# Kernel optimization log

Measured on AMD Instinct MI355X. Metric: run time of the kernel, lower is better.

## Reference

```python
import jax, jax.numpy as jnp
import numpy as np

N_DRUG = 2000
N_REL = 100
N_TAIL = 50000
E = 500_000
D = 128
SAMPLE = 64
BN_EPS = 1e-5


def setup_inputs() -> dict:
    key = jax.random.key(0)
    ks = jax.random.split(key, 12)
    xav = lambda k, shape: jax.random.normal(k, shape, jnp.float32) * np.float32(np.sqrt(2.0 / (shape[0] + shape[-1])))
    return {
        'drug_emb': xav(ks[0], (N_DRUG, D)),
        'rel_emb': xav(ks[1], (N_REL, D)),
        'tail_emb': xav(ks[2], (N_TAIL, D)),
        'w1': xav(ks[3], (D, D)),
        'b1': jnp.zeros((D,), jnp.float32),
        'w2': xav(ks[4], (D, D)),
        'b2': jnp.zeros((D,), jnp.float32),
        'fc2_w': xav(ks[5], (D, 2 * D)),
        'fc2_b': jnp.zeros((D,), jnp.float32),
        'gamma': jnp.ones((D,), jnp.float32),
        'beta': jnp.zeros((D,), jnp.float32),
        'x': jax.random.normal(ks[6], (N_DRUG, D), jnp.float32),
        'dkg_head': jnp.sort(jax.random.randint(ks[7], (E,), 0, N_DRUG, jnp.int32)),
        'dkg_rel': jax.random.randint(ks[8], (E,), 0, N_REL, jnp.int32),
        'dkg_tail': jax.random.randint(ks[9], (E,), 0, N_TAIL, jnp.int32),
        'sample_size': SAMPLE,
    }


def reference(drug_emb, rel_emb, tail_emb, w1, b1, w2, b2, fc2_w, fc2_b,
              gamma, beta, x, dkg_head, dkg_rel, dkg_tail, sample_size):
    n_drug, d = drug_emb.shape
    n_edges = dkg_head.shape[0]
    # per-edge semantic score: MLP(drug[h] * rel[r]) summed over feature dim
    had = drug_emb[dkg_head] * rel_emb[dkg_rel]            # [E, D]
    h = jax.nn.sigmoid(had @ w1.T + b1)                    # [E, D]
    score = jnp.sum(h @ w2.T + b2, axis=1, keepdims=True)  # [E, 1]
    temp = score * tail_emb[dkg_tail]                      # [E, D]
    # per-head sampling without replacement: keep at most sample_size edges
    # per drug (edges are sorted by head; rank = position within head group).
    starts = jnp.searchsorted(dkg_head, jnp.arange(n_drug, dtype=dkg_head.dtype))
    rank = jnp.arange(n_edges) - starts[dkg_head]
    keep = (rank < sample_size).astype(temp.dtype)[:, None]
    neigh = jax.ops.segment_sum(temp * keep, dkg_head, num_segments=n_drug)  # [N, D]
    # fullConnectionLayer2: Linear(2D -> D) + BatchNorm1d (training stats)
    concat = jnp.concatenate([drug_emb, neigh], axis=1)    # [N, 2D]
    out = concat @ fc2_w.T + fc2_b                         # [N, D]
    mean = jnp.mean(out, axis=0)
    var = jnp.var(out, axis=0)
    out = (out - mean) * jax.lax.rsqrt(var + BN_EPS) * gamma + beta
    return (out, x)
```

## Files before the change

### kernel.cpp

```cpp
#include <hip/hip_runtime.h>
#include <hip/hip_bf16.h>


#define D 128

typedef __attribute__((ext_vector_type(8))) short bf16x8;
typedef __attribute__((ext_vector_type(8))) unsigned short u16x8;
typedef __attribute__((ext_vector_type(4))) float f32x4;
typedef __attribute__((ext_vector_type(4))) unsigned short u16x4;

__device__ __forceinline__ unsigned short f2bf(float f) {
  union { float f; unsigned int u; } v; v.f = f;
  unsigned int r = v.u + 0x7FFFu + ((v.u >> 16) & 1u);
  return (unsigned short)(r >> 16);
}

__global__ void prep_kernel(const float* __restrict__ w1,
                            const float* __restrict__ w2,
                            const float* __restrict__ b2,
                            const float* __restrict__ drug_emb,
                            const float* __restrict__ fc2_w,
                            const float* __restrict__ x,
                            const int* __restrict__ head,
                            unsigned short* __restrict__ w1b,
                            unsigned short* __restrict__ drugb,
                            unsigned short* __restrict__ fc2wb,
                            int* __restrict__ starts,
                            float* __restrict__ w2s,
                            float* __restrict__ b2sum,
                            float* __restrict__ out_hi,
                            float* __restrict__ bnacc,
                            int* __restrict__ counter,
                            int E_total, int n_drug, int total) {
  int g = blockIdx.x * 256 + threadIdx.x;
  if (g < E_total) {
    int h1 = head[g];
    int h0 = (g == 0) ? -1 : head[g - 1];
    for (int d = h0 + 1; d <= h1; ++d) starts[d] = g;
    if (g == E_total - 1) {
      for (int d = h1 + 1; d <= n_drug; ++d) starts[d] = E_total;
    }
  }
  if (g < D * D) w1b[g] = f2bf(w1[g]);
  if (g < 2 * D * D) fc2wb[g] = f2bf(fc2_w[g]);
  if (g < n_drug * D) drugb[g] = f2bf(drug_emb[g]);
  if (g < total) out_hi[g] = x[g];
  if (g < 2 * D) bnacc[g] = 0.f;
  if (g == 2 * D) *counter = 0;
  if (g < D) {
    float s0=0.f,s1=0.f,s2=0.f,s3=0.f,s4=0.f,s5=0.f,s6=0.f,s7=0.f;
    #pragma unroll
    for (int j = 0; j < D; j += 8) {
      s0 += w2[(j+0)*D+g]; s1 += w2[(j+1)*D+g];
      s2 += w2[(j+2)*D+g]; s3 += w2[(j+3)*D+g];
      s4 += w2[(j+4)*D+g]; s5 += w2[(j+5)*D+g];
      s6 += w2[(j+6)*D+g]; s7 += w2[(j+7)*D+g];
    }
    w2s[g] = ((s0+s1)+(s2+s3))+((s4+s5)+(s6+s7));
  }
  if (g < 64) {
    float v = b2[g] + b2[g + 64];
    v += __shfl_xor(v, 1);  v += __shfl_xor(v, 2);  v += __shfl_xor(v, 4);
    v += __shfl_xor(v, 8);  v += __shfl_xor(v, 16); v += __shfl_xor(v, 32);
    if (g == 0) b2sum[0] = v;
  }
}

__global__ __launch_bounds__(256, 2) void edge_kernel(
    const float* __restrict__ drug_emb, const float* __restrict__ rel_emb,
    const float* __restrict__ tail_emb, const float* __restrict__ b1,
    const int* __restrict__ dkg_rel, const int* __restrict__ dkg_tail,
    const int* __restrict__ starts, const unsigned short* __restrict__ w1b,
    const float* __restrict__ w2s, const float* __restrict__ b2sum,
    const int* __restrict__ samp, unsigned short* __restrict__ neighb) {
  const int n = blockIdx.x;
  const int tid = threadIdx.x;
  const int w = tid >> 6, lane = tid & 63;
  const int fl = lane & 15, kh = lane >> 4;
  const int g = tid >> 5, l5 = tid & 31;

  __shared__ __align__(16) unsigned short hadb[64][136];
  __shared__ float scorePart[4][64];
  __shared__ float scoreL[64];
  __shared__ int   tails[64];
  __shared__ int   relIdx[64];
  float* gpart = (float*)&hadb[0][0];

  const int base = starts[n];
  const int end  = starts[n + 1];
  int ss = samp[0]; if (ss > 64) ss = 64;
  int cnt = end - base; if (cnt > ss) cnt = ss; if (cnt < 0) cnt = 0;

  if (tid < 64) {
    tails[tid]  = (tid < cnt) ? dkg_tail[base + tid] : 0;
    relIdx[tid] = (tid < cnt) ? dkg_rel[base + tid] : 0;
  }

  const f32x4 dr = *(const f32x4*)(drug_emb + (long)n * D + l5 * 4);

  bf16x8 bfr[2][4];
  float w2sr[2], b1r[2];
  #pragma unroll
  for (int jq = 0; jq < 2; ++jq) {
    int f = (w * 2 + jq) * 16 + fl;
    w2sr[jq] = w2s[f];
    b1r[jq]  = b1[f];
    #pragma unroll
    for (int kt = 0; kt < 4; ++kt)
      bfr[jq][kt] = *(const bf16x8*)(w1b + f * D + kt * 32 + kh * 8);
  }
  const float b2s = b2sum[0];

  __syncthreads();

  #pragma unroll
  for (int it = 0; it < 8; ++it) {
    int e = it * 8 + g;
    int r = relIdx[e];
    f32x4 rl = *(const f32x4*)(rel_emb + (long)r * D + l5 * 4);
    f32x4 v = dr * rl;
    u16x4 pk = { f2bf(v.x), f2bf(v.y), f2bf(v.z), f2bf(v.w) };
    *(u16x4*)&hadb[e][l5 * 4] = pk;
  }

  f32x4 trow[8];
  #pragma unroll
  for (int it = 0; it < 8; ++it) {
    int e = it * 8 + g;
    trow[it] = *(const f32x4*)(tail_emb + (long)tails[e] * D + l5 * 4);
  }

  __syncthreads();

  f32x4 acc[4][2];
  #pragma unroll
  for (int mt = 0; mt < 4; ++mt)
    #pragma unroll
    for (int jq = 0; jq < 2; ++jq)
      acc[mt][jq] = (f32x4){b1r[jq], b1r[jq], b1r[jq], b1r[jq]};

  #pragma unroll
  for (int kt = 0; kt < 4; ++kt) {
    bf16x8 af[4];
    #pragma unroll
    for (int mt = 0; mt < 4; ++mt)
      af[mt] = *(const bf16x8*)&hadb[mt * 16 + fl][kt * 32 + kh * 8];
    #pragma unroll
    for (int mt = 0; mt < 4; ++mt)
      #pragma unroll
      for (int jq = 0; jq < 2; ++jq)
        acc[mt][jq] = __builtin_amdgcn_mfma_f32_16x16x32_bf16(af[mt], bfr[jq][kt], acc[mt][jq], 0, 0, 0);
  }

  #pragma unroll
  for (int mt = 0; mt < 4; ++mt) {
    #pragma unroll
    for (int r = 0; r < 4; ++r) {
      float p = 0.f;
      #pragma unroll
      for (int jq = 0; jq < 2; ++jq) {
        float hh = 1.f / (1.f + __expf(-acc[mt][jq][r]));
        p += hh * w2sr[jq];
      }
      p += __shfl_xor(p, 1);
      p += __shfl_xor(p, 2);
      p += __shfl_xor(p, 4);
      p += __shfl_xor(p, 8);
      if (fl == 0) scorePart[w][mt * 16 + kh * 4 + r] = p;
    }
  }
  __syncthreads();

  if (tid < 64) {
    float sc = scorePart[0][tid] + scorePart[1][tid] + scorePart[2][tid] + scorePart[3][tid] + b2s;
    scoreL[tid] = (tid < cnt) ? sc : 0.f;
  }
  __syncthreads();

  f32x4 a = (f32x4){0.f, 0.f, 0.f, 0.f};
  #pragma unroll
  for (int it = 0; it < 8; ++it) {
    int e = it * 8 + g;
    float s = scoreL[e];
    a += trow[it] * s;
  }
  ((f32x4*)gpart)[g * 32 + l5] = a;
  __syncthreads();

  if (tid < D) {
    float s = 0.f;
    #pragma unroll
    for (int q = 0; q < 8; ++q) s += gpart[q * 128 + tid];
    neighb[(long)n * D + tid] = f2bf(s);
  }
}

__global__ __launch_bounds__(256, 1) void fc2bn_kernel(
    const unsigned short* __restrict__ drugb, const unsigned short* __restrict__ neighb,
    const unsigned short* __restrict__ fc2wb, const float* __restrict__ fc2_b,
    const float* __restrict__ gamma, const float* __restrict__ beta,
    float* __restrict__ bnacc, int* __restrict__ counter,
    float* __restrict__ out, int n_drug, int nblocks) {
  const int tid = threadIdx.x;
  const int w = tid >> 6, lane = tid & 63;
  const int fl = lane & 15, kh = lane >> 4;
  const int n0 = blockIdx.x * 64;

  __shared__ __align__(16) unsigned short asmem[64][264];

  #pragma unroll
  for (int it = 0; it < 8; ++it) {
    int c = it * 256 + tid;
    int row = c >> 5;
    int off = (c & 31) * 16;
    int gr = n0 + row;
    u16x8 v = (u16x8){0,0,0,0,0,0,0,0};
    if (gr < n_drug) {
      const unsigned short* src = (off < 256) ? (drugb + (long)gr * D + (off >> 1))
                                              : (neighb + (long)gr * D + ((off - 256) >> 1));
      v = *(const u16x8*)src;
    }
    *(u16x8*)((char*)&asmem[0][0] + row * 528 + off) = v;
  }

  bf16x8 bfr[2][8];
  float bjr[2];
  #pragma unroll
  for (int jq = 0; jq < 2; ++jq) {
    int f = (w * 2 + jq) * 16 + fl;
    bjr[jq] = fc2_b[f];
    #pragma unroll
    for (int kt = 0; kt < 8; ++kt)
      bfr[jq][kt] = *(const bf16x8*)(fc2wb + (long)f * 256 + kt * 32 + kh * 8);
  }
  __syncthreads();

  f32x4 acc[4][2];
  #pragma unroll
  for (int mt = 0; mt < 4; ++mt)
    #pragma unroll
    for (int jq = 0; jq < 2; ++jq)
      acc[mt][jq] = (f32x4){bjr[jq], bjr[jq], bjr[jq], bjr[jq]};

  #pragma unroll
  for (int kt = 0; kt < 8; ++kt) {
    bf16x8 af[4];
    #pragma unroll
    for (int mt = 0; mt < 4; ++mt)
      af[mt] = *(const bf16x8*)((char*)&asmem[0][0] + (mt * 16 + fl) * 528 + kt * 64 + kh * 16);
    #pragma unroll
    for (int mt = 0; mt < 4; ++mt)
      #pragma unroll
      for (int jq = 0; jq < 2; ++jq)
        acc[mt][jq] = __builtin_amdgcn_mfma_f32_16x16x32_bf16(af[mt], bfr[jq][kt], acc[mt][jq], 0, 0, 0);
  }

  #pragma unroll
  for (int jq = 0; jq < 2; ++jq) {
    int j = (w * 2 + jq) * 16 + fl;
    float s = 0.f, s2 = 0.f;
    #pragma unroll
    for (int mt = 0; mt < 4; ++mt) {
      #pragma unroll
      for (int r = 0; r < 4; ++r) {
        int grow = n0 + mt * 16 + kh * 4 + r;
        float v = acc[mt][jq][r];
        if (grow < n_drug) { s += v; s2 += v * v; }
      }
    }
    s  += __shfl_xor(s, 16);  s  += __shfl_xor(s, 32);
    s2 += __shfl_xor(s2, 16); s2 += __shfl_xor(s2, 32);
    if (kh == 0) {
      atomicAdd(&bnacc[j], s);
      atomicAdd(&bnacc[D + j], s2);
    }
  }

  __syncthreads();
  if (tid == 0) {
    __threadfence();
    atomicAdd(counter, 1);
    while (__hip_atomic_load(counter, __ATOMIC_ACQUIRE, __HIP_MEMORY_SCOPE_AGENT) < nblocks) {}
  }
  __syncthreads();

  #pragma unroll
  for (int jq = 0; jq < 2; ++jq) {
    int j = (w * 2 + jq) * 16 + fl;
    float s  = __hip_atomic_load(&bnacc[j],     __ATOMIC_RELAXED, __HIP_MEMORY_SCOPE_AGENT);
    float s2 = __hip_atomic_load(&bnacc[D + j], __ATOMIC_RELAXED, __HIP_MEMORY_SCOPE_AGENT);
    float mean = s / (float)n_drug;
    float var  = s2 / (float)n_drug - mean * mean;
    float inv  = rsqrtf(var + 1e-5f);
    float sc   = inv * gamma[j];
    float sh   = beta[j] - mean * sc;
    #pragma unroll
    for (int mt = 0; mt < 4; ++mt) {
      #pragma unroll
      for (int r = 0; r < 4; ++r) {
        int grow = n0 + mt * 16 + kh * 4 + r;
        if (grow < n_drug)
          out[(long)grow * D + j] = acc[mt][jq][r] * sc + sh;
      }
    }
  }
}

extern "C" void kernel_launch(void* const* d_in, const int* in_sizes, int n_in,
                              void* d_out, int out_size, void* d_ws, size_t ws_size,
                              hipStream_t stream) {
  const float* drug_emb = (const float*)d_in[0];
  const float* rel_emb  = (const float*)d_in[1];
  const float* tail_emb = (const float*)d_in[2];
  const float* w1       = (const float*)d_in[3];
  const float* b1       = (const float*)d_in[4];
  const float* w2       = (const float*)d_in[5];
  const float* b2       = (const float*)d_in[6];
  const float* fc2_w    = (const float*)d_in[7];
  const float* fc2_b    = (const float*)d_in[8];
  const float* gamma    = (const float*)d_in[9];
  const float* beta     = (const float*)d_in[10];
  const float* x        = (const float*)d_in[11];
  const int*   dkg_head = (const int*)d_in[12];
  const int*   dkg_rel  = (const int*)d_in[13];
  const int*   dkg_tail = (const int*)d_in[14];
  const int*   samp     = (const int*)d_in[15];

  const int n_drug = in_sizes[0] / D;
  const int E      = in_sizes[12];
  float* out = (float*)d_out;
  const int total = out_size / 2;

  char* ws = (char*)d_ws;
  int*            starts  = (int*)(ws + 0);
  unsigned short* w1b     = (unsigned short*)(ws + 8192);
  float*          w2s     = (float*)(ws + 40960);
  float*          b2sum   = (float*)(ws + 41472);
  unsigned short* fc2wb   = (unsigned short*)(ws + 49152);
  unsigned short* drugb   = (unsigned short*)(ws + 131072);
  unsigned short* neighb  = (unsigned short*)(ws + 655360);
  float*          bnacc   = (float*)(ws + 1179648);
  int*            counter = (int*)(ws + 1180672);

  const int nbf = (n_drug + 63) / 64;

  hipLaunchKernelGGL(prep_kernel, dim3((E + 256) / 256), dim3(256), 0, stream,
                     w1, w2, b2, drug_emb, fc2_w, x, dkg_head,
                     w1b, drugb, fc2wb, starts, w2s, b2sum, out + total,
                     bnacc, counter, E, n_drug, total);
  hipLaunchKernelGGL(edge_kernel, dim3(n_drug), dim3(256), 0, stream,
                     drug_emb, rel_emb, tail_emb, b1, dkg_rel, dkg_tail,
                     starts, w1b, w2s, b2sum, samp, neighb);
  hipLaunchKernelGGL(fc2bn_kernel, dim3(nbf), dim3(256), 0, stream,
                     drugb, neighb, fc2wb, fc2_b, gamma, beta,
                     bnacc, counter, out, n_drug, nbf);
}
```

Before: 41.69 us.

## Fuse edge and fc2+batchnorm kernels via grid-wide atomic barrier

Merges the per-drug edge aggregation kernel and the fc2+BatchNorm kernel into one launch. The last NF blocks (one per 32 drugs) wait on a global atomic counter until every block has written its neighbour row, then run the fc2 MFMA and BN reduction with a second counter barrier. This removes one kernel launch and its gap. It also halves the fc2 tile to 32 rows and streams weight fragments per k-step instead of holding them all in registers. The risk is deadlock if the waiting blocks occupy resources that unfinished blocks need, and the tail blocks sit idle while they spin.

```diff
diff --git a/kernel.cpp b/kernel.cpp
--- a/kernel.cpp
+++ b/kernel.cpp
@@ -30,7 +30,7 @@
                             float* __restrict__ b2sum,
                             float* __restrict__ out_hi,
                             float* __restrict__ bnacc,
-                            int* __restrict__ counter,
+                            int* __restrict__ counters,
                             int E_total, int n_drug, int total) {
   int g = blockIdx.x * 256 + threadIdx.x;
   if (g < E_total) {
@@ -46,7 +46,7 @@
   if (g < n_drug * D) drugb[g] = f2bf(drug_emb[g]);
   if (g < total) out_hi[g] = x[g];
   if (g < 2 * D) bnacc[g] = 0.f;
-  if (g == 2 * D) *counter = 0;
+  if (g == 2 * D) { counters[0] = 0; counters[1] = 0; }
   if (g < D) {
     float s0=0.f,s1=0.f,s2=0.f,s3=0.f,s4=0.f,s5=0.f,s6=0.f,s7=0.f;
     #pragma unroll
@@ -66,25 +66,31 @@
   }
 }
 
-__global__ __launch_bounds__(256, 2) void edge_kernel(
+__global__ __launch_bounds__(256, 2) void mega_kernel(
     const float* __restrict__ drug_emb, const float* __restrict__ rel_emb,
     const float* __restrict__ tail_emb, const float* __restrict__ b1,
     const int* __restrict__ dkg_rel, const int* __restrict__ dkg_tail,
     const int* __restrict__ starts, const unsigned short* __restrict__ w1b,
     const float* __restrict__ w2s, const float* __restrict__ b2sum,
-    const int* __restrict__ samp, unsigned short* __restrict__ neighb) {
+    const int* __restrict__ samp, unsigned short* __restrict__ neighb,
+    const unsigned short* __restrict__ drugb,
+    const unsigned short* __restrict__ fc2wb, const float* __restrict__ fc2_b,
+    const float* __restrict__ gamma, const float* __restrict__ beta,
+    float* __restrict__ bnacc, int* __restrict__ counters,
+    float* __restrict__ out, int n_drug) {
   const int n = blockIdx.x;
   const int tid = threadIdx.x;
   const int w = tid >> 6, lane = tid & 63;
   const int fl = lane & 15, kh = lane >> 4;
   const int g = tid >> 5, l5 = tid & 31;
 
-  __shared__ __align__(16) unsigned short hadb[64][136];
-  __shared__ float scorePart[4][64];
-  __shared__ float scoreL[64];
-  __shared__ int   tails[64];
-  __shared__ int   relIdx[64];
-  float* gpart = (float*)&hadb[0][0];
+  __shared__ __align__(16) char smem[19456];
+  unsigned short (*hadb)[136]    = (unsigned short(*)[136])smem;
+  float (*scorePart)[64]         = (float(*)[64])(smem + 17408);
+  float* scoreL                  = (float*)(smem + 18432);
+  int*   tails                   = (int*)(smem + 18688);
+  int*   relIdx                  = (int*)(smem + 18944);
+  float* gpart                   = (float*)smem;
 
   const int base = starts[n];
   const int end  = starts[n + 1];
@@ -193,23 +199,28 @@
     for (int q = 0; q < 8; ++q) s += gpart[q * 128 + tid];
     neighb[(long)n * D + tid] = f2bf(s);
   }
-}
-
-__global__ __launch_bounds__(256, 1) void fc2bn_kernel(
-    const unsigned short* __restrict__ drugb, const unsigned short* __restrict__ neighb,
-    const unsigned short* __restrict__ fc2wb, const float* __restrict__ fc2_b,
-    const float* __restrict__ gamma, const float* __restrict__ beta,
-    float* __restrict__ bnacc, int* __restrict__ counter,
-    float* __restrict__ out, int n_drug, int nblocks) {
-  const int tid = threadIdx.x;
-  const int w = tid >> 6, lane = tid & 63;
-  const int fl = lane & 15, kh = lane >> 4;
-  const int n0 = blockIdx.x * 64;
-
-  __shared__ __align__(16) unsigned short asmem[64][264];
-
-  #pragma unroll
-  for (int it = 0; it < 8; ++it) {
+
+  const int NF = (n_drug + 31) >> 5;
+  const int nblk = (int)gridDim.x;
+  __syncthreads();
+  if (tid == 0) {
+    __threadfence();
+    atomicAdd(&counters[0], 1);
+  }
+  if (n < nblk - NF) return;
+
+  if (tid == 0) {
+    while (__hip_atomic_load(&counters[0], __ATOMIC_ACQUIRE, __HIP_MEMORY_SCOPE_AGENT) < nblk) {}
+    __threadfence();
+  }
+  __syncthreads();
+
+  const int fb = n - (nblk - NF);
+  const int n0 = fb * 32;
+  unsigned short (*asmem)[264] = (unsigned short(*)[264])smem;
+
+  #pragma unroll
+  for (int it = 0; it < 4; ++it) {
     int c = it * 256 + tid;
     int row = c >> 5;
     int off = (c & 31) * 16;
@@ -223,36 +234,33 @@
     *(u16x8*)((char*)&asmem[0][0] + row * 528 + off) = v;
   }
 
-  bf16x8 bfr[2][8];
   float bjr[2];
   #pragma unroll
-  for (int jq = 0; jq < 2; ++jq) {
-    int f = (w * 2 + jq) * 16 + fl;
-    bjr[jq] = fc2_b[f];
-    #pragma unroll
-    for (int kt = 0; kt < 8; ++kt)
-      bfr[jq][kt] = *(const bf16x8*)(fc2wb + (long)f * 256 + kt * 32 + kh * 8);
-  }
-  __syncthreads();
-
-  f32x4 acc[4][2];
-  #pragma unroll
-  for (int mt = 0; mt < 4; ++mt)
+  for (int jq = 0; jq < 2; ++jq) bjr[jq] = fc2_b[(w * 2 + jq) * 16 + fl];
+  __syncthreads();
+
+  f32x4 facc[2][2];
+  #pragma unroll
+  for (int mt = 0; mt < 2; ++mt)
     #pragma unroll
     for (int jq = 0; jq < 2; ++jq)
-      acc[mt][jq] = (f32x4){bjr[jq], bjr[jq], bjr[jq], bjr[jq]};
+      facc[mt][jq] = (f32x4){bjr[jq], bjr[jq], bjr[jq], bjr[jq]};
 
   #pragma unroll
   for (int kt = 0; kt < 8; ++kt) {
-    bf16x8 af[4];
-    #pragma unroll
-    for (int mt = 0; mt < 4; ++mt)
+    bf16x8 fbfr[2];
+    #pragma unroll
+    for (int jq = 0; jq < 2; ++jq)
+      fbfr[jq] = *(const bf16x8*)(fc2wb + (long)((w * 2 + jq) * 16 + fl) * 256 + kt * 32 + kh * 8);
+    bf16x8 af[2];
+    #pragma unroll
+    for (int mt = 0; mt < 2; ++mt)
       af[mt] = *(const bf16x8*)((char*)&asmem[0][0] + (mt * 16 + fl) * 528 + kt * 64 + kh * 16);
     #pragma unroll
-    for (int mt = 0; mt < 4; ++mt)
+    for (int mt = 0; mt < 2; ++mt)
       #pragma unroll
       for (int jq = 0; jq < 2; ++jq)
-        acc[mt][jq] = __builtin_amdgcn_mfma_f32_16x16x32_bf16(af[mt], bfr[jq][kt], acc[mt][jq], 0, 0, 0);
+        facc[mt][jq] = __builtin_amdgcn_mfma_f32_16x16x32_bf16(af[mt], fbfr[jq], facc[mt][jq], 0, 0, 0);
   }
 
   #pragma unroll
@@ -260,11 +268,11 @@
     int j = (w * 2 + jq) * 16 + fl;
     float s = 0.f, s2 = 0.f;
     #pragma unroll
-    for (int mt = 0; mt < 4; ++mt) {
+    for (int mt = 0; mt < 2; ++mt) {
       #pragma unroll
       for (int r = 0; r < 4; ++r) {
         int grow = n0 + mt * 16 + kh * 4 + r;
-        float v = acc[mt][jq][r];
+        float v = facc[mt][jq][r];
         if (grow < n_drug) { s += v; s2 += v * v; }
       }
     }
@@ -279,8 +287,9 @@
   __syncthreads();
   if (tid == 0) {
     __threadfence();
-    atomicAdd(counter, 1);
-    while (__hip_atomic_load(counter, __ATOMIC_ACQUIRE, __HIP_MEMORY_SCOPE_AGENT) < nblocks) {}
+    atomicAdd(&counters[1], 1);
+    while (__hip_atomic_load(&counters[1], __ATOMIC_ACQUIRE, __HIP_MEMORY_SCOPE_AGENT) < NF) {}
+    __threadfence();
   }
   __syncthreads();
 
@@ -295,12 +304,12 @@
     float sc   = inv * gamma[j];
     float sh   = beta[j] - mean * sc;
     #pragma unroll
-    for (int mt = 0; mt < 4; ++mt) {
+    for (int mt = 0; mt < 2; ++mt) {
       #pragma unroll
       for (int r = 0; r < 4; ++r) {
         int grow = n0 + mt * 16 + kh * 4 + r;
         if (grow < n_drug)
-          out[(long)grow * D + j] = acc[mt][jq][r] * sc + sh;
+          out[(long)grow * D + j] = facc[mt][jq][r] * sc + sh;
       }
     }
   }
@@ -332,26 +341,23 @@
   const int total = out_size / 2;
 
   char* ws = (char*)d_ws;
-  int*            starts  = (int*)(ws + 0);
-  unsigned short* w1b     = (unsigned short*)(ws + 8192);
-  float*          w2s     = (float*)(ws + 40960);
-  float*          b2sum   = (float*)(ws + 41472);
-  unsigned short* fc2wb   = (unsigned short*)(ws + 49152);
-  unsigned short* drugb   = (unsigned short*)(ws + 131072);
-  unsigned short* neighb  = (unsigned short*)(ws + 655360);
-  float*          bnacc   = (float*)(ws + 1179648);
-  int*            counter = (int*)(ws + 1180672);
-
-  const int nbf = (n_drug + 63) / 64;
+  int*            starts   = (int*)(ws + 0);
+  unsigned short* w1b      = (unsigned short*)(ws + 8192);
+  float*          w2s      = (float*)(ws + 40960);
+  float*          b2sum    = (float*)(ws + 41472);
+  unsigned short* fc2wb    = (unsigned short*)(ws + 49152);
+  unsigned short* drugb    = (unsigned short*)(ws + 131072);
+  unsigned short* neighb   = (unsigned short*)(ws + 655360);
+  float*          bnacc    = (float*)(ws + 1179648);
+  int*            counters = (int*)(ws + 1180672);
 
   hipLaunchKernelGGL(prep_kernel, dim3((E + 256) / 256), dim3(256), 0, stream,
                      w1, w2, b2, drug_emb, fc2_w, x, dkg_head,
                      w1b, drugb, fc2wb, starts, w2s, b2sum, out + total,
-                     bnacc, counter, E, n_drug, total);
-  hipLaunchKernelGGL(edge_kernel, dim3(n_drug), dim3(256), 0, stream,
+                     bnacc, counters, E, n_drug, total);
+  hipLaunchKernelGGL(mega_kernel, dim3(n_drug), dim3(256), 0, stream,
                      drug_emb, rel_emb, tail_emb, b1, dkg_rel, dkg_tail,
-                     starts, w1b, w2s, b2sum, samp, neighb);
-  hipLaunchKernelGGL(fc2bn_kernel, dim3(nbf), dim3(256), 0, stream,
-                     drugb, neighb, fc2wb, fc2_b, gamma, beta,
-                     bnacc, counter, out, n_drug, nbf);
+                     starts, w1b, w2s, b2sum, samp, neighb,
+                     drugb, fc2wb, fc2_b, gamma, beta,
+                     bnacc, counters, out, n_drug);
 }
```

Measured after the change: 92.36 us. 122% more time.

## Eliminate prep kernel by fusing setup work into edge and fc2 kernels

Applied to the files above, without the earlier changes.

Removes the separate prep launch that scanned all 500k head entries, converted weights to bf16 and copied x. Each edge block now binary-searches its own segment bounds, converts w1 to bf16 and reduces w2 columns on the fly, and copies its row of x. The fc2 kernel converts drug_emb and fc2_w from fp32 as it loads them. This saves one launch and a full pass over the edge array, but every block now repeats the weight conversion and w2 reduction. The bnacc and counter reset moves into edge block 0, which relies on stream ordering before fc2bn runs.

```diff
diff --git a/kernel.cpp b/kernel.cpp
--- a/kernel.cpp
+++ b/kernel.cpp
@@ -15,64 +15,15 @@
   return (unsigned short)(r >> 16);
 }
 
-__global__ void prep_kernel(const float* __restrict__ w1,
-                            const float* __restrict__ w2,
-                            const float* __restrict__ b2,
-                            const float* __restrict__ drug_emb,
-                            const float* __restrict__ fc2_w,
-                            const float* __restrict__ x,
-                            const int* __restrict__ head,
-                            unsigned short* __restrict__ w1b,
-                            unsigned short* __restrict__ drugb,
-                            unsigned short* __restrict__ fc2wb,
-                            int* __restrict__ starts,
-                            float* __restrict__ w2s,
-                            float* __restrict__ b2sum,
-                            float* __restrict__ out_hi,
-                            float* __restrict__ bnacc,
-                            int* __restrict__ counter,
-                            int E_total, int n_drug, int total) {
-  int g = blockIdx.x * 256 + threadIdx.x;
-  if (g < E_total) {
-    int h1 = head[g];
-    int h0 = (g == 0) ? -1 : head[g - 1];
-    for (int d = h0 + 1; d <= h1; ++d) starts[d] = g;
-    if (g == E_total - 1) {
-      for (int d = h1 + 1; d <= n_drug; ++d) starts[d] = E_total;
-    }
-  }
-  if (g < D * D) w1b[g] = f2bf(w1[g]);
-  if (g < 2 * D * D) fc2wb[g] = f2bf(fc2_w[g]);
-  if (g < n_drug * D) drugb[g] = f2bf(drug_emb[g]);
-  if (g < total) out_hi[g] = x[g];
-  if (g < 2 * D) bnacc[g] = 0.f;
-  if (g == 2 * D) *counter = 0;
-  if (g < D) {
-    float s0=0.f,s1=0.f,s2=0.f,s3=0.f,s4=0.f,s5=0.f,s6=0.f,s7=0.f;
-    #pragma unroll
-    for (int j = 0; j < D; j += 8) {
-      s0 += w2[(j+0)*D+g]; s1 += w2[(j+1)*D+g];
-      s2 += w2[(j+2)*D+g]; s3 += w2[(j+3)*D+g];
-      s4 += w2[(j+4)*D+g]; s5 += w2[(j+5)*D+g];
-      s6 += w2[(j+6)*D+g]; s7 += w2[(j+7)*D+g];
-    }
-    w2s[g] = ((s0+s1)+(s2+s3))+((s4+s5)+(s6+s7));
-  }
-  if (g < 64) {
-    float v = b2[g] + b2[g + 64];
-    v += __shfl_xor(v, 1);  v += __shfl_xor(v, 2);  v += __shfl_xor(v, 4);
-    v += __shfl_xor(v, 8);  v += __shfl_xor(v, 16); v += __shfl_xor(v, 32);
-    if (g == 0) b2sum[0] = v;
-  }
-}
-
 __global__ __launch_bounds__(256, 2) void edge_kernel(
     const float* __restrict__ drug_emb, const float* __restrict__ rel_emb,
-    const float* __restrict__ tail_emb, const float* __restrict__ b1,
-    const int* __restrict__ dkg_rel, const int* __restrict__ dkg_tail,
-    const int* __restrict__ starts, const unsigned short* __restrict__ w1b,
-    const float* __restrict__ w2s, const float* __restrict__ b2sum,
-    const int* __restrict__ samp, unsigned short* __restrict__ neighb) {
+    const float* __restrict__ tail_emb, const float* __restrict__ w1,
+    const float* __restrict__ b1, const float* __restrict__ w2,
+    const float* __restrict__ b2, const float* __restrict__ x,
+    const int* __restrict__ dkg_head, const int* __restrict__ dkg_rel,
+    const int* __restrict__ dkg_tail, const int* __restrict__ samp,
+    unsigned short* __restrict__ neighb, float* __restrict__ out_hi,
+    float* __restrict__ bnacc, int* __restrict__ counters, int E) {
   const int n = blockIdx.x;
   const int tid = threadIdx.x;
   const int w = tid >> 6, lane = tid & 63;
@@ -84,34 +35,84 @@
   __shared__ float scoreL[64];
   __shared__ int   tails[64];
   __shared__ int   relIdx[64];
-  float* gpart = (float*)&hadb[0][0];
-
-  const int base = starts[n];
-  const int end  = starts[n + 1];
+  __shared__ float b2sL;
+  __shared__ int   baseL[2];
+  float* gpart  = (float*)&hadb[0][0];
+  float* w2part = (float*)&scorePart[0][0];
+
+  if (n == 0) {
+    if (tid < 2 * D) bnacc[tid] = 0.f;
+    if (tid == 0) { counters[0] = 0; counters[1] = 0; }
+  }
+
+  if (tid < 2) {
+    int target = n + tid;
+    int lo = 0, hi = E;
+    while (lo < hi) { int mid = (lo + hi) >> 1; if (dkg_head[mid] < target) lo = mid + 1; else hi = mid; }
+    baseL[tid] = lo;
+  }
+
+  if (tid < D) out_hi[(long)n * D + tid] = x[(long)n * D + tid];
+
+  if (tid < 64) {
+    float v = b2[tid] + b2[tid + 64];
+    v += __shfl_xor(v, 1);  v += __shfl_xor(v, 2);  v += __shfl_xor(v, 4);
+    v += __shfl_xor(v, 8);  v += __shfl_xor(v, 16); v += __shfl_xor(v, 32);
+    if (tid == 0) b2sL = v;
+  }
+
+  const f32x4 dr = *(const f32x4*)(drug_emb + (long)n * D + l5 * 4);
   int ss = samp[0]; if (ss > 64) ss = 64;
-  int cnt = end - base; if (cnt > ss) cnt = ss; if (cnt < 0) cnt = 0;
+
+  __syncthreads();
+
+  const int base = baseL[0];
+  int cnt = baseL[1] - base; if (cnt > ss) cnt = ss; if (cnt < 0) cnt = 0;
 
   if (tid < 64) {
     tails[tid]  = (tid < cnt) ? dkg_tail[base + tid] : 0;
     relIdx[tid] = (tid < cnt) ? dkg_rel[base + tid] : 0;
   }
 
-  const f32x4 dr = *(const f32x4*)(drug_emb + (long)n * D + l5 * 4);
+  {
+    const int f = tid & 127, jh = tid >> 7;
+    const float* p = w2 + (long)(jh * 64) * D + f;
+    float s0 = 0.f, s1 = 0.f, s2 = 0.f, s3 = 0.f;
+    #pragma unroll
+    for (int j = 0; j < 64; j += 4) {
+      s0 += p[(j + 0) * D]; s1 += p[(j + 1) * D];
+      s2 += p[(j + 2) * D]; s3 += p[(j + 3) * D];
+    }
+    w2part[jh * 128 + f] = (s0 + s1) + (s2 + s3);
+  }
 
   bf16x8 bfr[2][4];
-  float w2sr[2], b1r[2];
+  float b1r[2];
   #pragma unroll
   for (int jq = 0; jq < 2; ++jq) {
     int f = (w * 2 + jq) * 16 + fl;
-    w2sr[jq] = w2s[f];
-    b1r[jq]  = b1[f];
-    #pragma unroll
-    for (int kt = 0; kt < 4; ++kt)
-      bfr[jq][kt] = *(const bf16x8*)(w1b + f * D + kt * 32 + kh * 8);
-  }
-  const float b2s = b2sum[0];
-
-  __syncthreads();
+    b1r[jq] = b1[f];
+    #pragma unroll
+    for (int kt = 0; kt < 4; ++kt) {
+      const float* src = w1 + (long)f * D + kt * 32 + kh * 8;
+      f32x4 a0 = *(const f32x4*)src;
+      f32x4 a1 = *(const f32x4*)(src + 4);
+      bfr[jq][kt] = (bf16x8){(short)f2bf(a0.x), (short)f2bf(a0.y),
+                             (short)f2bf(a0.z), (short)f2bf(a0.w),
+                             (short)f2bf(a1.x), (short)f2bf(a1.y),
+                             (short)f2bf(a1.z), (short)f2bf(a1.w)};
+    }
+  }
+
+  __syncthreads();
+
+  float w2sr[2];
+  #pragma unroll
+  for (int jq = 0; jq < 2; ++jq) {
+    int f = (w * 2 + jq) * 16 + fl;
+    w2sr[jq] = w2part[f] + w2part[128 + f];
+  }
+  const float b2s = b2sL;
 
   #pragma unroll
   for (int it = 0; it < 8; ++it) {
@@ -196,10 +197,10 @@
 }
 
 __global__ __launch_bounds__(256, 1) void fc2bn_kernel(
-    const unsigned short* __restrict__ drugb, const unsigned short* __restrict__ neighb,
-    const unsigned short* __restrict__ fc2wb, const float* __restrict__ fc2_b,
+    const float* __restrict__ drug_emb, const unsigned short* __restrict__ neighb,
+    const float* __restrict__ fc2_w, const float* __restrict__ fc2_b,
     const float* __restrict__ gamma, const float* __restrict__ beta,
-    float* __restrict__ bnacc, int* __restrict__ counter,
+    float* __restrict__ bnacc, int* __restrict__ counters,
     float* __restrict__ out, int n_drug, int nblocks) {
   const int tid = threadIdx.x;
   const int w = tid >> 6, lane = tid & 63;
@@ -216,9 +217,15 @@
     int gr = n0 + row;
     u16x8 v = (u16x8){0,0,0,0,0,0,0,0};
     if (gr < n_drug) {
-      const unsigned short* src = (off < 256) ? (drugb + (long)gr * D + (off >> 1))
-                                              : (neighb + (long)gr * D + ((off - 256) >> 1));
-      v = *(const u16x8*)src;
+      if (off < 256) {
+        const float* s = drug_emb + (long)gr * D + (off >> 1);
+        f32x4 a0 = *(const f32x4*)s;
+        f32x4 a1 = *(const f32x4*)(s + 4);
+        v = (u16x8){f2bf(a0.x), f2bf(a0.y), f2bf(a0.z), f2bf(a0.w),
+                    f2bf(a1.x), f2bf(a1.y), f2bf(a1.z), f2bf(a1.w)};
+      } else {
+        v = *(const u16x8*)(neighb + (long)gr * D + ((off - 256) >> 1));
+      }
     }
     *(u16x8*)((char*)&asmem[0][0] + row * 528 + off) = v;
   }
@@ -230,8 +237,15 @@
     int f = (w * 2 + jq) * 16 + fl;
     bjr[jq] = fc2_b[f];
     #pragma unroll
-    for (int kt = 0; kt < 8; ++kt)
-      bfr[jq][kt] = *(const bf16x8*)(fc2wb + (long)f * 256 + kt * 32 + kh * 8);
+    for (int kt = 0; kt < 8; ++kt) {
+      const float* src = fc2_w + (long)f * 256 + kt * 32 + kh * 8;
+      f32x4 a0 = *(const f32x4*)src;
+      f32x4 a1 = *(const f32x4*)(src + 4);
+      bfr[jq][kt] = (bf16x8){(short)f2bf(a0.x), (short)f2bf(a0.y),
+                             (short)f2bf(a0.z), (short)f2bf(a0.w),
+                             (short)f2bf(a1.x), (short)f2bf(a1.y),
+                             (short)f2bf(a1.z), (short)f2bf(a1.w)};
+    }
   }
   __syncthreads();
 
@@ -279,8 +293,8 @@
   __syncthreads();
   if (tid == 0) {
     __threadfence();
-    atomicAdd(counter, 1);
-    while (__hip_atomic_load(counter, __ATOMIC_ACQUIRE, __HIP_MEMORY_SCOPE_AGENT) < nblocks) {}
+    atomicAdd(&counters[0], 1);
+    while (__hip_atomic_load(&counters[0], __ATOMIC_ACQUIRE, __HIP_MEMORY_SCOPE_AGENT) < nblocks) {}
   }
   __syncthreads();
 
@@ -332,26 +346,17 @@
   const int total = out_size / 2;
 
   char* ws = (char*)d_ws;
-  int*            starts  = (int*)(ws + 0);
-  unsigned short* w1b     = (unsigned short*)(ws + 8192);
-  float*          w2s     = (float*)(ws + 40960);
-  float*          b2sum   = (float*)(ws + 41472);
-  unsigned short* fc2wb   = (unsigned short*)(ws + 49152);
-  unsigned short* drugb   = (unsigned short*)(ws + 131072);
-  unsigned short* neighb  = (unsigned short*)(ws + 655360);
-  float*          bnacc   = (float*)(ws + 1179648);
-  int*            counter = (int*)(ws + 1180672);
+  unsigned short* neighb   = (unsigned short*)(ws + 0);
+  float*          bnacc    = (float*)(ws + 524288);
+  int*            counters = (int*)(ws + 525312);
 
   const int nbf = (n_drug + 63) / 64;
 
-  hipLaunchKernelGGL(prep_kernel, dim3((E + 256) / 256), dim3(256), 0, stream,
-                     w1, w2, b2, drug_emb, fc2_w, x, dkg_head,
-                     w1b, drugb, fc2wb, starts, w2s, b2sum, out + total,
-                     bnacc, counter, E, n_drug, total);
   hipLaunchKernelGGL(edge_kernel, dim3(n_drug), dim3(256), 0, stream,
-                     drug_emb, rel_emb, tail_emb, b1, dkg_rel, dkg_tail,
-                     starts, w1b, w2s, b2sum, samp, neighb);
+                     drug_emb, rel_emb, tail_emb, w1, b1, w2, b2, x,
+                     dkg_head, dkg_rel, dkg_tail, samp,
+                     neighb, out + total, bnacc, counters, E);
   hipLaunchKernelGGL(fc2bn_kernel, dim3(nbf), dim3(256), 0, stream,
-                     drugb, neighb, fc2wb, fc2_b, gamma, beta,
-                     bnacc, counter, out, n_drug, nbf);
+                     drug_emb, neighb, fc2_w, fc2_b, gamma, beta,
+                     bnacc, counters, out, n_drug, nbf);
 }
```

Result: slower. 67.05 us (+60.8%).
